# Kernel tuning notes

Hardware: AMD Instinct MI355X
Metric: run time of the kernel (lower is better)

The kernel has to match this reference:

```python
import jax, jax.numpy as jnp
import numpy as np

B, S, D = 4, 1024, 2048
H, KVH, HD = 32, 8, 64
N_REP = H // KVH  # 4
ROPE_THETA = 1000000.0


def _rope_tables(seq_len, head_dim, theta):
    inv_freq = 1.0 / (theta ** (np.arange(0, head_dim, 2, dtype=np.float32) / head_dim))
    t = np.arange(seq_len, dtype=np.float32)
    freqs = np.outer(t, inv_freq)                      # (S, HD/2)
    emb = np.concatenate([freqs, freqs], axis=-1)      # (S, HD)
    return jnp.asarray(np.cos(emb)), jnp.asarray(np.sin(emb))


def setup_inputs() -> dict:
    key = jax.random.key(0)
    kx, kq, kk, kv, ko = jax.random.split(key, 5)
    cos, sin = _rope_tables(S, HD, ROPE_THETA)
    s = 0.02
    return {
        "x": jax.random.normal(kx, (B, S, D), jnp.float32),
        "cos": cos,
        "sin": sin,
        "Wq": jax.random.normal(kq, (D, H * HD), jnp.float32) * s,
        "Wk": jax.random.normal(kk, (D, KVH * HD), jnp.float32) * s,
        "Wv": jax.random.normal(kv, (D, KVH * HD), jnp.float32) * s,
        "Wo": jax.random.normal(ko, (H * HD, D), jnp.float32) * s,
    }


def _rotate_half(t):
    t1, t2 = jnp.split(t, 2, axis=-1)
    return jnp.concatenate([-t2, t1], axis=-1)


def reference(x, cos, sin, Wq, Wk, Wv, Wo):
    # projections
    q = (x @ Wq).reshape(B, S, H, HD)      # (b, s, h, d)
    k = (x @ Wk).reshape(B, S, KVH, HD)
    v = (x @ Wv).reshape(B, S, KVH, HD)

    # RoPE: cos/sin (s, d) broadcast over heads (unsqueeze_dim=1 -> (s,1,d))
    c = cos[:, None, :]
    sn = sin[:, None, :]
    q = q * c + _rotate_half(q) * sn
    k = k * c + _rotate_half(k) * sn

    # GQA attention without physically repeating KV:
    # q grouped as (b, kvh, n_rep, s, d); repeat_kv '(h r)' maps q head g*n_rep+r -> kv head g
    qg = q.transpose(0, 2, 1, 3).reshape(B, KVH, N_REP, S, HD)
    kt = k.transpose(0, 2, 1, 3)  # (b, kvh, s, d)
    vt = v.transpose(0, 2, 1, 3)

    scale = 1.0 / jnp.sqrt(jnp.asarray(HD, x.dtype))
    scores = jnp.einsum('bgrqd,bgkd->bgrqk', qg, kt) * scale  # (b, kvh, rep, s, s)
    probs = jax.nn.softmax(scores, axis=-1)
    out = jnp.einsum('bgrqk,bgkd->bgrqd', probs, vt)           # (b, kvh, rep, s, d)

    out = out.reshape(B, H, S, HD).transpose(0, 2, 1, 3).reshape(B, S, H * HD)
    return out @ Wo
```

## Files before the change

### kernel.cpp

```cpp
#include <hip/hip_runtime.h>

typedef unsigned short u16;
typedef __attribute__((ext_vector_type(8))) __bf16 bf16x8;
typedef __attribute__((ext_vector_type(4))) _Float16 f16x4;
typedef __attribute__((ext_vector_type(4))) float f32x4;

#define BB 4
#define SS 1024
#define DD 2048
#define HH 32
#define KVHN 8
#define HDIM 64

__device__ __forceinline__ u16 f2b(float f) {
    union { float f; unsigned u; } v; v.f = f;
    unsigned r = v.u + 0x7FFFu + ((v.u >> 16) & 1u);
    return (u16)(r >> 16);
}
__device__ __forceinline__ float b2f(u16 h) {
    union { unsigned u; float f; } v; v.u = ((unsigned)h) << 16; return v.f;
}

__device__ __forceinline__ f32x4 mfma16(bf16x8 a, bf16x8 b, f32x4 c) {
    return __builtin_amdgcn_mfma_f32_16x16x32_bf16(a, b, c, 0, 0, 0);
}

#define MFMA_F16_16(a, b, c) __builtin_amdgcn_mfma_f32_16x16x16f16(a, b, c, 0, 0, 0)

__device__ __forceinline__ void async_cp16(const void* g, void* l) {
    __builtin_amdgcn_global_load_lds((__attribute__((address_space(1))) void*)g,
                                     (__attribute__((address_space(3))) void*)l,
                                     16, 0, 0);
}

__device__ __forceinline__ f16x4 pack4_f16(float p0, float p1, float p2, float p3) {
    union { unsigned u[2]; f16x4 v; } pu;
    pu.u[0] = __builtin_bit_cast(unsigned, __builtin_amdgcn_cvt_pkrtz(p0, p1));
    pu.u[1] = __builtin_bit_cast(unsigned, __builtin_amdgcn_cvt_pkrtz(p2, p3));
    return pu.v;
}

__global__ __launch_bounds__(256) void cast_x_kernel(const float* __restrict__ x,
                                                     u16* __restrict__ xb) {
    int i = (blockIdx.x * 256 + threadIdx.x) * 4;
    float4 v = *(const float4*)(x + i);
    unsigned r0 = (unsigned)f2b(v.x) | ((unsigned)f2b(v.y) << 16);
    unsigned r1 = (unsigned)f2b(v.z) | ((unsigned)f2b(v.w) << 16);
    *(uint2*)(xb + i) = make_uint2(r0, r1);
}

__global__ __launch_bounds__(256) void wtrans_all_kernel(const float* __restrict__ Wq,
                                                         const float* __restrict__ Wk,
                                                         const float* __restrict__ Wv,
                                                         const float* __restrict__ Wo,
                                                         u16* __restrict__ Wqkvt,
                                                         u16* __restrict__ Wot) {
    __shared__ float tile[32][33];
    int z = blockIdx.z;
    const float* W = (z == 0) ? Wq : (z == 1) ? Wk : (z == 2) ? Wv : Wo;
    int N = (z == 1 || z == 2) ? 512 : 2048;
    int n_off = (z == 1) ? 2048 : (z == 2) ? 2560 : 0;
    u16* Wt = (z == 3) ? Wot : Wqkvt;
    int n0 = blockIdx.x * 32;
    if (n0 >= N) return;
    int k0 = blockIdx.y * 32;
    int tid = threadIdx.x;
    int nj = tid & 31;
    int ki = tid >> 5;
#pragma unroll
    for (int it = 0; it < 4; it++) {
        int kk = it * 8 + ki;
        tile[kk][nj] = W[(size_t)(k0 + kk) * N + n0 + nj];
    }
    __syncthreads();
#pragma unroll
    for (int it = 0; it < 4; it++) {
        int nn = it * 8 + ki;
        Wt[(size_t)(n0 + nn + n_off) * 2048 + k0 + nj] = f2b(tile[nj][nn]);
    }
}

template <int OUT_BF16>
__device__ __forceinline__ void gemm_bt_body(const u16* __restrict__ A,
                                             const u16* __restrict__ Bt,
                                             void* __restrict__ Cv,
                                             int M, int N, int K) {
    __shared__ __align__(16) u16 As[128 * 64];
    __shared__ __align__(16) u16 Bs[128 * 64];
    const int tid = threadIdx.x;
    const int lane = tid & 63;
    const int w = tid >> 6;
    const int m0 = blockIdx.y * 128;
    const int n0 = blockIdx.x * 128;
    const int wm = (w >> 1) * 64;
    const int wn = (w & 1) * 64;
    const int lr = lane & 15;
    const int lg = lane >> 4;
    const int lq = lg * 4;

    const f32x4 zero4 = {0.f, 0.f, 0.f, 0.f};
    f32x4 acc[4][4];
#pragma unroll
    for (int i = 0; i < 4; i++)
#pragma unroll
        for (int j = 0; j < 4; j++) acc[i][j] = zero4;

    for (int k0 = 0; k0 < K; k0 += 64) {
#pragma unroll
        for (int sh = 0; sh < 4; sh++) {
            int i_lin = sh * 256 + tid;
            int row = i_lin >> 3;
            int c = i_lin & 7;
            int cs = c ^ (row & 7);
            async_cp16(A + (size_t)(m0 + row) * K + k0 + cs * 8, As + sh * 2048 + w * 512);
            async_cp16(Bt + (size_t)(n0 + row) * K + k0 + cs * 8, Bs + sh * 2048 + w * 512);
        }
        __syncthreads();
#pragma unroll
        for (int kb = 0; kb < 2; kb++) {
            bf16x8 af[4], bfr[4];
#pragma unroll
            for (int mi = 0; mi < 4; mi++) {
                int r = wm + mi * 16 + lr;
                af[mi] = *(const bf16x8*)(As + r * 64 + (((kb * 4 + lg) ^ (r & 7)) * 8));
            }
#pragma unroll
            for (int ni = 0; ni < 4; ni++) {
                int r = wn + ni * 16 + lr;
                bfr[ni] = *(const bf16x8*)(Bs + r * 64 + (((kb * 4 + lg) ^ (r & 7)) * 8));
            }
#pragma unroll
            for (int mi = 0; mi < 4; mi++)
#pragma unroll
                for (int ni = 0; ni < 4; ni++)
                    acc[mi][ni] = mfma16(af[mi], bfr[ni], acc[mi][ni]);
        }
        __syncthreads();
    }

    if (OUT_BF16) {
        u16* C = (u16*)Cv;
#pragma unroll
        for (int mi = 0; mi < 4; mi++)
#pragma unroll
            for (int ni = 0; ni < 4; ni++)
#pragma unroll
                for (int i = 0; i < 4; i++) {
                    int r = m0 + wm + mi * 16 + lq + i;
                    int c = n0 + wn + ni * 16 + lr;
                    C[(size_t)r * N + c] = f2b(acc[mi][ni][i]);
                }
    } else {
        float* C = (float*)Cv;
#pragma unroll
        for (int mi = 0; mi < 4; mi++)
#pragma unroll
            for (int ni = 0; ni < 4; ni++)
#pragma unroll
                for (int i = 0; i < 4; i++) {
                    int r = m0 + wm + mi * 16 + lq + i;
                    int c = n0 + wn + ni * 16 + lr;
                    C[(size_t)r * N + c] = acc[mi][ni][i];
                }
    }
}

__global__ __launch_bounds__(256) void gemm_qkv(const u16* __restrict__ A,
                                                const u16* __restrict__ Bt,
                                                void* __restrict__ Cv,
                                                int M, int N, int K) {
    gemm_bt_body<1>(A, Bt, Cv, M, N, K);
}

__global__ __launch_bounds__(256) void gemm_out(const u16* __restrict__ A,
                                                const u16* __restrict__ Bt,
                                                void* __restrict__ Cv,
                                                int M, int N, int K) {
    gemm_bt_body<0>(A, Bt, Cv, M, N, K);
}

__global__ __launch_bounds__(256) void rope_kernel(const u16* __restrict__ QKV,
                                                   const float* __restrict__ cosT,
                                                   const float* __restrict__ sinT,
                                                   u16* __restrict__ Qh,
                                                   u16* __restrict__ Kh) {
    const float QSC = 0.125f * 1.44269504088896f;
    int idx = blockIdx.x * 256 + threadIdx.x;
    int d = idx & 31;
    int t = idx >> 5;
    int hh = t % 40;
    int row = t / 40;
    int s = row & (SS - 1);
    int b = row >> 10;
    float c = cosT[s * HDIM + d];
    float sn = sinT[s * HDIM + d];
    if (hh < 32) {
        const u16* src = QKV + (size_t)row * 3072 + hh * 64 + d;
        float x1 = b2f(src[0]), x2 = b2f(src[32]);
        u16* dst = Qh + ((size_t)(b * HH + hh) * SS + s) * 64 + d;
        dst[0] = f2b((x1 * c - x2 * sn) * QSC);
        dst[32] = f2b((x2 * c + x1 * sn) * QSC);
    } else {
        int g = hh - 32;
        const u16* src = QKV + (size_t)row * 3072 + 2048 + g * 64 + d;
        float x1 = b2f(src[0]), x2 = b2f(src[32]);
        u16* dst = Kh + ((size_t)(b * KVHN + g) * SS + s) * 64 + d;
        dst[0] = f2b(x1 * c - x2 * sn);
        dst[32] = f2b(x2 * c + x1 * sn);
    }
}

__global__ __launch_bounds__(256) void vtrans_kernel(const u16* __restrict__ QKV,
                                                     u16* __restrict__ Vt) {
    __shared__ u16 tile[64][65];
    int blk = blockIdx.x;
    int st = blk & 15;
    int t2 = blk >> 4;
    int g = t2 & 7;
    int b = t2 >> 3;
    int tid = threadIdx.x;
    int cj = tid & 63;
    int ri = tid >> 6;
    const u16* src = QKV + ((size_t)(b * SS + st * 64)) * 3072 + 2560 + g * 64;
#pragma unroll
    for (int it = 0; it < 16; it++) {
        int s_i = it * 4 + ri;
        tile[s_i][cj] = src[(size_t)s_i * 3072 + cj];
    }
    __syncthreads();
    int cp = ((cj >> 2) & 3) * 16 + ((cj >> 4) & 3) * 4 + (cj & 3);
    u16* dst = Vt + ((size_t)(b * KVHN + g) * HDIM) * SS + st * 64;
#pragma unroll
    for (int it = 0; it < 16; it++) {
        int hd_i = it * 4 + ri;
        _Float16 hv = (_Float16)b2f(tile[cj][hd_i]);
        union { _Float16 h; u16 u; } cv; cv.h = hv;
        dst[(size_t)hd_i * SS + cp] = cv.u;
    }
}

__global__ __launch_bounds__(256) void flash_kernel(const u16* __restrict__ Qh,
                                                    const u16* __restrict__ Kh,
                                                    const u16* __restrict__ Vt,
                                                    u16* __restrict__ Attn) {
    __shared__ __align__(16) u16 Kls[2][4096];
    __shared__ __align__(16) u16 Vls[2][4096];
    const int tid = threadIdx.x;
    const int lane = tid & 63;
    const int w = tid >> 6;
    const int qt = blockIdx.x;
    const int g = blockIdx.y;
    const int b = blockIdx.z;
    const int h = g * 4 + w;
    const int lr = lane & 15;
    const int lg = lane >> 4;
    const int lk8 = lg * 8;
    const int lq = lg * 4;

    const u16* Qbase = Qh + ((size_t)(b * HH + h) * SS + qt * 64) * HDIM;
    bf16x8 qb[4][2];
#pragma unroll
    for (int j = 0; j < 4; j++) {
        qb[j][0] = *(const bf16x8*)(Qbase + (size_t)(j * 16 + lr) * HDIM + lk8);
        qb[j][1] = *(const bf16x8*)(Qbase + (size_t)(j * 16 + lr) * HDIM + 32 + lk8);
    }

    const u16* Kbase = Kh + (size_t)(b * KVHN + g) * SS * HDIM;
    const u16* Vbase = Vt + (size_t)(b * KVHN + g) * HDIM * SS;

    const int r0 = tid >> 3;
    const int c0 = tid & 7;

    const f32x4 zero4 = {0.f, 0.f, 0.f, 0.f};
    const f32x4 initS = {-4.f, -4.f, -4.f, -4.f};
    f32x4 o[4][4];
    float lsum[4] = {0.f, 0.f, 0.f, 0.f};
#pragma unroll
    for (int j = 0; j < 4; j++)
#pragma unroll
        for (int i = 0; i < 4; i++) o[j][i] = zero4;

#define STAGE(kt, p)                                                              \
    {                                                                             \
        _Pragma("unroll") for (int sh = 0; sh < 2; sh++) {                        \
            int rr = r0 + sh * 32;                                                \
            int cs = c0 ^ (rr & 7);                                               \
            async_cp16(Kbase + (size_t)((kt) + rr) * HDIM + cs * 8,               \
                       &Kls[p][sh * 2048 + w * 512]);                             \
            async_cp16(Vbase + (size_t)rr * SS + (kt) + cs * 8,                   \
                       &Vls[p][sh * 2048 + w * 512]);                             \
        }                                                                         \
    }

    STAGE(0, 0);
    __syncthreads();

    for (int t = 0; t < 16; t++) {
        const int p = t & 1;
        if (t < 15) STAGE((t + 1) * 64, p ^ 1);

#pragma unroll
        for (int nt = 0; nt < 4; nt++) {
            const int R = nt * 16 + lr;
            const u16* kr = &Kls[p][R * 64];
            bf16x8 kb0 = *(const bf16x8*)(kr + ((lg ^ (R & 7)) * 8));
            bf16x8 kb1 = *(const bf16x8*)(kr + (((4 + lg) ^ (R & 7)) * 8));

            f32x4 s[4];
#pragma unroll
            for (int j = 0; j < 4; j++) {
                f32x4 a = initS;
                a = mfma16(kb0, qb[j][0], a);
                a = mfma16(kb1, qb[j][1], a);
                s[j] = a;
            }

            f16x4 va[4];
#pragma unroll
            for (int hdt = 0; hdt < 4; hdt++) {
                const int R2 = hdt * 16 + lr;
                va[hdt] = *(const f16x4*)(&Vls[p][R2 * 64 + (((2 * lg + (nt >> 1)) ^ (R2 & 7)) * 8) + (nt & 1) * 4]);
            }

#pragma unroll
            for (int j = 0; j < 4; j++) {
                float p0 = __builtin_amdgcn_exp2f(s[j][0]);
                float p1 = __builtin_amdgcn_exp2f(s[j][1]);
                float p2 = __builtin_amdgcn_exp2f(s[j][2]);
                float p3 = __builtin_amdgcn_exp2f(s[j][3]);
                lsum[j] += (p0 + p1) + (p2 + p3);
                f16x4 pb = pack4_f16(p0, p1, p2, p3);
#pragma unroll
                for (int hdt = 0; hdt < 4; hdt++)
                    o[j][hdt] = MFMA_F16_16(va[hdt], pb, o[j][hdt]);
            }
        }
        __syncthreads();
    }

#pragma unroll
    for (int j = 0; j < 4; j++) {
        float su = lsum[j];
        su += __shfl_xor(su, 16);
        su += __shfl_xor(su, 32);
        float inv = 1.f / su;
        u16* Ob = Attn + ((size_t)(b * SS + qt * 64 + j * 16 + lr)) * 2048 + h * 64;
#pragma unroll
        for (int hdt = 0; hdt < 4; hdt++) {
            unsigned r0p = (unsigned)f2b(o[j][hdt][0] * inv) | ((unsigned)f2b(o[j][hdt][1] * inv) << 16);
            unsigned r1p = (unsigned)f2b(o[j][hdt][2] * inv) | ((unsigned)f2b(o[j][hdt][3] * inv) << 16);
            *(uint2*)(Ob + hdt * 16 + lq) = make_uint2(r0p, r1p);
        }
    }
}

extern "C" void kernel_launch(void* const* d_in, const int* in_sizes, int n_in,
                              void* d_out, int out_size, void* d_ws, size_t ws_size,
                              hipStream_t stream) {
    (void)in_sizes; (void)n_in; (void)out_size; (void)ws_size;
    const float* x = (const float*)d_in[0];
    const float* cosT = (const float*)d_in[1];
    const float* sinT = (const float*)d_in[2];
    const float* Wq = (const float*)d_in[3];
    const float* Wk = (const float*)d_in[4];
    const float* Wv = (const float*)d_in[5];
    const float* Wo = (const float*)d_in[6];
    float* out = (float*)d_out;

    char* ws = (char*)d_ws;
    u16* Xb    = (u16*)(ws);
    u16* Wqkvt = (u16*)(ws + 16777216);
    u16* Wot   = (u16*)(ws + 29360128);
    u16* QKV   = (u16*)(ws + 37748736);
    u16* Qh    = (u16*)(ws + 62914560);
    u16* Kh    = (u16*)(ws + 79691776);
    u16* Vt    = (u16*)(ws + 83886080);
    u16* Attn  = (u16*)(ws + 88080384);

    cast_x_kernel<<<8192, 256, 0, stream>>>(x, Xb);
    wtrans_all_kernel<<<dim3(64, 64, 4), 256, 0, stream>>>(Wq, Wk, Wv, Wo, Wqkvt, Wot);

    gemm_qkv<<<dim3(24, 32), 256, 0, stream>>>(Xb, Wqkvt, (void*)QKV, 4096, 3072, 2048);

    rope_kernel<<<20480, 256, 0, stream>>>(QKV, cosT, sinT, Qh, Kh);
    vtrans_kernel<<<512, 256, 0, stream>>>(QKV, Vt);

    flash_kernel<<<dim3(16, 8, 4), 256, 0, stream>>>(Qh, Kh, Vt, Attn);

    gemm_out<<<dim3(16, 32), 256, 0, stream>>>(Attn, Wot, (void*)out, 4096, 2048, 2048);
}
```

Baseline: 313.4 us.

## Use 16x16x32 f16 MFMA for PV with permuted K layout and smaller query tiles

The PV product now uses the wider 16x16x32 f16 MFMA, so each step consumes 32 keys. To match the operand layout, the K rows are permuted in the rope kernel and the V column permutation is dropped. The query tile per block is halved from 64 to 32 rows, which doubles the grid to 1024 blocks, and launch bounds are raised to target 4 blocks per CU. This trades fewer MFMA issues and more parallelism for reloading K/V tiles twice as often per query row.

```diff
diff --git a/kernel.cpp b/kernel.cpp
--- a/kernel.cpp
+++ b/kernel.cpp
@@ -3,6 +3,7 @@
 typedef unsigned short u16;
 typedef __attribute__((ext_vector_type(8))) __bf16 bf16x8;
 typedef __attribute__((ext_vector_type(4))) _Float16 f16x4;
+typedef __attribute__((ext_vector_type(8))) _Float16 f16x8;
 typedef __attribute__((ext_vector_type(4))) float f32x4;
 
 #define BB 4
@@ -24,8 +25,9 @@
 __device__ __forceinline__ f32x4 mfma16(bf16x8 a, bf16x8 b, f32x4 c) {
     return __builtin_amdgcn_mfma_f32_16x16x32_bf16(a, b, c, 0, 0, 0);
 }
-
-#define MFMA_F16_16(a, b, c) __builtin_amdgcn_mfma_f32_16x16x16f16(a, b, c, 0, 0, 0)
+__device__ __forceinline__ f32x4 mfma16h(f16x8 a, f16x8 b, f32x4 c) {
+    return __builtin_amdgcn_mfma_f32_16x16x32_f16(a, b, c, 0, 0, 0);
+}
 
 __device__ __forceinline__ void async_cp16(const void* g, void* l) {
     __builtin_amdgcn_global_load_lds((__attribute__((address_space(1))) void*)g,
@@ -33,10 +35,12 @@
                                      16, 0, 0);
 }
 
-__device__ __forceinline__ f16x4 pack4_f16(float p0, float p1, float p2, float p3) {
-    union { unsigned u[2]; f16x4 v; } pu;
-    pu.u[0] = __builtin_bit_cast(unsigned, __builtin_amdgcn_cvt_pkrtz(p0, p1));
-    pu.u[1] = __builtin_bit_cast(unsigned, __builtin_amdgcn_cvt_pkrtz(p2, p3));
+__device__ __forceinline__ f16x8 pack8_f16(const float* p) {
+    union { unsigned u[4]; f16x8 v; } pu;
+    pu.u[0] = __builtin_bit_cast(unsigned, __builtin_amdgcn_cvt_pkrtz(p[0], p[1]));
+    pu.u[1] = __builtin_bit_cast(unsigned, __builtin_amdgcn_cvt_pkrtz(p[2], p[3]));
+    pu.u[2] = __builtin_bit_cast(unsigned, __builtin_amdgcn_cvt_pkrtz(p[4], p[5]));
+    pu.u[3] = __builtin_bit_cast(unsigned, __builtin_amdgcn_cvt_pkrtz(p[6], p[7]));
     return pu.v;
 }
 
@@ -204,7 +208,9 @@
         int g = hh - 32;
         const u16* src = QKV + (size_t)row * 3072 + 2048 + g * 64 + d;
         float x1 = b2f(src[0]), x2 = b2f(src[32]);
-        u16* dst = Kh + ((size_t)(b * KVHN + g) * SS + s) * 64 + d;
+        int rr = s & 7;
+        int kpos = (s & ~31) + ((rr >= 4) ? 16 : 0) + ((s >> 3) & 3) * 4 + (rr & 3);
+        u16* dst = Kh + ((size_t)(b * KVHN + g) * SS + kpos) * 64 + d;
         dst[0] = f2b(x1 * c - x2 * sn);
         dst[32] = f2b(x2 * c + x1 * sn);
     }
@@ -228,21 +234,20 @@
         tile[s_i][cj] = src[(size_t)s_i * 3072 + cj];
     }
     __syncthreads();
-    int cp = ((cj >> 2) & 3) * 16 + ((cj >> 4) & 3) * 4 + (cj & 3);
     u16* dst = Vt + ((size_t)(b * KVHN + g) * HDIM) * SS + st * 64;
 #pragma unroll
     for (int it = 0; it < 16; it++) {
         int hd_i = it * 4 + ri;
         _Float16 hv = (_Float16)b2f(tile[cj][hd_i]);
         union { _Float16 h; u16 u; } cv; cv.h = hv;
-        dst[(size_t)hd_i * SS + cp] = cv.u;
-    }
-}
-
-__global__ __launch_bounds__(256) void flash_kernel(const u16* __restrict__ Qh,
-                                                    const u16* __restrict__ Kh,
-                                                    const u16* __restrict__ Vt,
-                                                    u16* __restrict__ Attn) {
+        dst[(size_t)hd_i * SS + cj] = cv.u;
+    }
+}
+
+__global__ __launch_bounds__(256, 4) void flash_kernel(const u16* __restrict__ Qh,
+                                                       const u16* __restrict__ Kh,
+                                                       const u16* __restrict__ Vt,
+                                                       u16* __restrict__ Attn) {
     __shared__ __align__(16) u16 Kls[2][4096];
     __shared__ __align__(16) u16 Vls[2][4096];
     const int tid = threadIdx.x;
@@ -257,10 +262,10 @@
     const int lk8 = lg * 8;
     const int lq = lg * 4;
 
-    const u16* Qbase = Qh + ((size_t)(b * HH + h) * SS + qt * 64) * HDIM;
-    bf16x8 qb[4][2];
-#pragma unroll
-    for (int j = 0; j < 4; j++) {
+    const u16* Qbase = Qh + ((size_t)(b * HH + h) * SS + qt * 32) * HDIM;
+    bf16x8 qb[2][2];
+#pragma unroll
+    for (int j = 0; j < 2; j++) {
         qb[j][0] = *(const bf16x8*)(Qbase + (size_t)(j * 16 + lr) * HDIM + lk8);
         qb[j][1] = *(const bf16x8*)(Qbase + (size_t)(j * 16 + lr) * HDIM + 32 + lk8);
     }
@@ -273,10 +278,10 @@
 
     const f32x4 zero4 = {0.f, 0.f, 0.f, 0.f};
     const f32x4 initS = {-4.f, -4.f, -4.f, -4.f};
-    f32x4 o[4][4];
-    float lsum[4] = {0.f, 0.f, 0.f, 0.f};
-#pragma unroll
-    for (int j = 0; j < 4; j++)
+    f32x4 o[2][4];
+    float lsum[2] = {0.f, 0.f};
+#pragma unroll
+    for (int j = 0; j < 2; j++)
 #pragma unroll
         for (int i = 0; i < 4; i++) o[j][i] = zero4;
 
@@ -300,51 +305,56 @@
         if (t < 15) STAGE((t + 1) * 64, p ^ 1);
 
 #pragma unroll
-        for (int nt = 0; nt < 4; nt++) {
-            const int R = nt * 16 + lr;
-            const u16* kr = &Kls[p][R * 64];
-            bf16x8 kb0 = *(const bf16x8*)(kr + ((lg ^ (R & 7)) * 8));
-            bf16x8 kb1 = *(const bf16x8*)(kr + (((4 + lg) ^ (R & 7)) * 8));
-
-            f32x4 s[4];
-#pragma unroll
-            for (int j = 0; j < 4; j++) {
-                f32x4 a = initS;
-                a = mfma16(kb0, qb[j][0], a);
-                a = mfma16(kb1, qb[j][1], a);
-                s[j] = a;
+        for (int c = 0; c < 2; c++) {
+            f32x4 s[2][2];
+#pragma unroll
+            for (int halfi = 0; halfi < 2; halfi++) {
+                const int R = c * 32 + halfi * 16 + lr;
+                const u16* kr = &Kls[p][R * 64];
+                bf16x8 kb0 = *(const bf16x8*)(kr + ((lg ^ (R & 7)) * 8));
+                bf16x8 kb1 = *(const bf16x8*)(kr + (((4 + lg) ^ (R & 7)) * 8));
+#pragma unroll
+                for (int j = 0; j < 2; j++) {
+                    f32x4 a = initS;
+                    a = mfma16(kb0, qb[j][0], a);
+                    a = mfma16(kb1, qb[j][1], a);
+                    s[halfi][j] = a;
+                }
             }
 
-            f16x4 va[4];
+            f16x8 va[4];
 #pragma unroll
             for (int hdt = 0; hdt < 4; hdt++) {
                 const int R2 = hdt * 16 + lr;
-                va[hdt] = *(const f16x4*)(&Vls[p][R2 * 64 + (((2 * lg + (nt >> 1)) ^ (R2 & 7)) * 8) + (nt & 1) * 4]);
+                va[hdt] = *(const f16x8*)(&Vls[p][R2 * 64 + (((c * 4 + lg) ^ (R2 & 7)) * 8)]);
             }
 
 #pragma unroll
-            for (int j = 0; j < 4; j++) {
-                float p0 = __builtin_amdgcn_exp2f(s[j][0]);
-                float p1 = __builtin_amdgcn_exp2f(s[j][1]);
-                float p2 = __builtin_amdgcn_exp2f(s[j][2]);
-                float p3 = __builtin_amdgcn_exp2f(s[j][3]);
-                lsum[j] += (p0 + p1) + (p2 + p3);
-                f16x4 pb = pack4_f16(p0, p1, p2, p3);
+            for (int j = 0; j < 2; j++) {
+                float pv[8];
+#pragma unroll
+                for (int r = 0; r < 4; r++) {
+                    pv[r] = __builtin_amdgcn_exp2f(s[0][j][r]);
+                    pv[4 + r] = __builtin_amdgcn_exp2f(s[1][j][r]);
+                }
+                lsum[j] += ((pv[0] + pv[1]) + (pv[2] + pv[3])) +
+                           ((pv[4] + pv[5]) + (pv[6] + pv[7]));
+                f16x8 pb = pack8_f16(pv);
 #pragma unroll
                 for (int hdt = 0; hdt < 4; hdt++)
-                    o[j][hdt] = MFMA_F16_16(va[hdt], pb, o[j][hdt]);
+                    o[j][hdt] = mfma16h(va[hdt], pb, o[j][hdt]);
             }
         }
         __syncthreads();
     }
 
 #pragma unroll
-    for (int j = 0; j < 4; j++) {
+    for (int j = 0; j < 2; j++) {
         float su = lsum[j];
         su += __shfl_xor(su, 16);
         su += __shfl_xor(su, 32);
         float inv = 1.f / su;
-        u16* Ob = Attn + ((size_t)(b * SS + qt * 64 + j * 16 + lr)) * 2048 + h * 64;
+        u16* Ob = Attn + ((size_t)(b * SS + qt * 32 + j * 16 + lr)) * 2048 + h * 64;
 #pragma unroll
         for (int hdt = 0; hdt < 4; hdt++) {
             unsigned r0p = (unsigned)f2b(o[j][hdt][0] * inv) | ((unsigned)f2b(o[j][hdt][1] * inv) << 16);
@@ -385,7 +395,7 @@
     rope_kernel<<<20480, 256, 0, stream>>>(QKV, cosT, sinT, Qh, Kh);
     vtrans_kernel<<<512, 256, 0, stream>>>(QKV, Vt);
 
-    flash_kernel<<<dim3(16, 8, 4), 256, 0, stream>>>(Qh, Kh, Vt, Attn);
+    flash_kernel<<<dim3(32, 8, 4), 256, 0, stream>>>(Qh, Kh, Vt, Attn);
 
     gemm_out<<<dim3(16, 32), 256, 0, stream>>>(Attn, Wot, (void*)out, 4096, 2048, 2048);
 }
```

After: 282.2 us. 1.11x faster.
